# Optimization experiments

Hardware: AMD Instinct MI355X
Metric: run time of the kernel (lower is better)

## Reference

```python
import jax, jax.numpy as jnp
import numpy as np

# Allpass biquad coefficients (torchaudio.functional.allpass_biquad semantics)
SAMPLE_RATE = 16000
CENTRAL_FREQ = 4000.0
Q = 0.707

def _allpass_coeffs(sample_rate, central_freq, q):
    w0 = 2.0 * np.pi * central_freq / sample_rate
    alpha = np.sin(w0) / (2.0 * q)
    cos_w0 = np.cos(w0)
    b0 = 1.0 - alpha
    b1 = -2.0 * cos_w0
    b2 = 1.0 + alpha
    a0 = 1.0 + alpha
    a1 = -2.0 * cos_w0
    a2 = 1.0 - alpha
    # normalize by a0 (as torchaudio.biquad does)
    return (np.float32(b0 / a0), np.float32(b1 / a0), np.float32(b2 / a0),
            np.float32(a1 / a0), np.float32(a2 / a0))

B0, B1, B2, A1, A2 = _allpass_coeffs(SAMPLE_RATE, CENTRAL_FREQ, Q)


def setup_inputs() -> dict:
    key = jax.random.key(0)
    x = jax.random.normal(key, (64, 1, 480000), dtype=jnp.float32)
    return {"x": x}


def _biquad(x):
    # x: [B, 1, T] -> y: [B, 1, T]
    B, C, T = x.shape
    xt = jnp.transpose(x[:, 0, :])  # [T, B] for time-major scan

    def step(carry, xn):
        x1, x2, y1, y2 = carry
        yn = B0 * xn + B1 * x1 + B2 * x2 - A1 * y1 - A2 * y2
        return (xn, x1, yn, y1), yn

    z = jnp.zeros((B,), dtype=x.dtype)
    _, yt = jax.lax.scan(step, (z, z, z, z), xt)
    return jnp.transpose(yt)[:, None, :]  # back to [B, 1, T]


def reference(x):
    return _biquad(x)
```

## Files before the change

kernel.cpp:

```cpp
#include <hip/hip_runtime.h>
#include <cmath>

#define T_LEN   480000
#define BATCH   64
#define CHUNK   16
#define WARM    32
#define TPB     256
#define TS      (TPB * CHUNK)
#define TPR     ((T_LEN + TS - 1) / TS)
#define NLOAD_MAX (TS + WARM)
#define LDS_SLOTS (NLOAD_MAX + ((NLOAD_MAX >> 5) << 2))

__device__ __forceinline__ int slot4(int i) { return i + ((i >> 5) << 2); }

#define STEP(XN, YN)                                            \
    {                                                           \
        float u_ = fmaf(B0, (XN), fmaf(B1, x1, B2 * x2));       \
        (YN) = fmaf(-A1, y1, fmaf(-A2, y2, u_));                \
        x2 = x1; x1 = (XN); y2 = y1; y1 = (YN);                 \
    }

__global__ __launch_bounds__(TPB) void allpass_kernel(
    const float* __restrict__ x, float* __restrict__ y,
    float B0, float B1, float B2, float A1, float A2)
{
    __shared__ __align__(16) float lds[LDS_SLOTS];
    const int tid  = threadIdx.x;
    const int row  = blockIdx.x / TPR;
    const int tb   = blockIdx.x % TPR;
    const int sbase = tb * TS;
    const int ns   = min(TS, T_LEN - sbase);
    const float* __restrict__ xr = x + (size_t)row * T_LEN + sbase;
    float* __restrict__ yr       = y + (size_t)row * T_LEN + sbase;

    const int nload = ns + WARM;
    for (int i4 = tid * 4; i4 < nload; i4 += TPB * 4) {
        float4 v;
        if (tb == 0 && i4 < WARM) {
            v = make_float4(0.f, 0.f, 0.f, 0.f);
        } else {
            v = *(const float4*)(xr - WARM + i4);
        }
        *(float4*)&lds[slot4(i4)] = v;
    }
    __syncthreads();

    float4 yq[CHUNK / 4];
    const int ls = tid * CHUNK;
    const bool active = (ls < ns);
    if (active) {
        float x1 = 0.f, x2 = 0.f, y1 = 0.f, y2 = 0.f;
        #pragma unroll
        for (int t4 = 0; t4 < WARM; t4 += 4) {
            float4 xv = *(const float4*)&lds[slot4(ls + t4)];
            float t;
            STEP(xv.x, t); STEP(xv.y, t); STEP(xv.z, t); STEP(xv.w, t);
        }
        #pragma unroll
        for (int t4 = 0; t4 < CHUNK; t4 += 4) {
            float4 xv = *(const float4*)&lds[slot4(ls + WARM + t4)];
            float4 yv;
            STEP(xv.x, yv.x); STEP(xv.y, yv.y);
            STEP(xv.z, yv.z); STEP(xv.w, yv.w);
            yq[t4 / 4] = yv;
        }
    }
    __syncthreads();

    if (active) {
        #pragma unroll
        for (int t4 = 0; t4 < CHUNK; t4 += 4)
            *(float4*)&lds[slot4(ls + t4)] = yq[t4 / 4];
    }
    __syncthreads();

    for (int i4 = tid * 4; i4 < ns; i4 += TPB * 4) {
        float4 v = *(const float4*)&lds[slot4(i4)];
        *(float4*)(yr + i4) = v;
    }
}

extern "C" void kernel_launch(void* const* d_in, const int* in_sizes, int n_in,
                              void* d_out, int out_size, void* d_ws, size_t ws_size,
                              hipStream_t stream) {
    const float* x = (const float*)d_in[0];
    float* y = (float*)d_out;

    const double sample_rate = 16000.0, central_freq = 4000.0, Q = 0.707;
    const double w0 = 2.0 * M_PI * central_freq / sample_rate;
    const double alpha = sin(w0) / (2.0 * Q);
    const double cw = cos(w0);
    const double a0 = 1.0 + alpha;
    const float B0 = (float)((1.0 - alpha) / a0);
    const float B1 = (float)((-2.0 * cw) / a0);
    const float B2 = (float)((1.0 + alpha) / a0);
    const float A1 = (float)((-2.0 * cw) / a0);
    const float A2 = (float)((1.0 - alpha) / a0);

    const int blocks = BATCH * TPR;
    allpass_kernel<<<blocks, TPB, 0, stream>>>(x, y, B0, B1, B2, A1, A2);
}
```

Baseline: 216.4 us.

## Halve warm-up length, batch global loads, store outputs directly to global

```diff
diff --git a/kernel.cpp b/kernel.cpp
--- a/kernel.cpp
+++ b/kernel.cpp
@@ -4,11 +4,12 @@
 #define T_LEN   480000
 #define BATCH   64
 #define CHUNK   16
-#define WARM    32
+#define WARM    16
 #define TPB     256
 #define TS      (TPB * CHUNK)
 #define TPR     ((T_LEN + TS - 1) / TS)
 #define NLOAD_MAX (TS + WARM)
+#define NITER   ((NLOAD_MAX + TPB * 4 - 1) / (TPB * 4))
 #define LDS_SLOTS (NLOAD_MAX + ((NLOAD_MAX >> 5) << 2))
 
 __device__ __forceinline__ int slot4(int i) { return i + ((i >> 5) << 2); }
@@ -32,23 +33,29 @@
     const int ns   = min(TS, T_LEN - sbase);
     const float* __restrict__ xr = x + (size_t)row * T_LEN + sbase;
     float* __restrict__ yr       = y + (size_t)row * T_LEN + sbase;
+    const int nload = ns + WARM;
 
-    const int nload = ns + WARM;
-    for (int i4 = tid * 4; i4 < nload; i4 += TPB * 4) {
-        float4 v;
-        if (tb == 0 && i4 < WARM) {
-            v = make_float4(0.f, 0.f, 0.f, 0.f);
-        } else {
-            v = *(const float4*)(xr - WARM + i4);
+    float4 vbuf[NITER];
+    #pragma unroll
+    for (int j = 0; j < NITER; ++j) {
+        const int i4 = tid * 4 + j * (TPB * 4);
+        if (i4 < nload) {
+            if (tb == 0 && i4 < WARM)
+                vbuf[j] = make_float4(0.f, 0.f, 0.f, 0.f);
+            else
+                vbuf[j] = *(const float4*)(xr - WARM + i4);
         }
-        *(float4*)&lds[slot4(i4)] = v;
+    }
+    #pragma unroll
+    for (int j = 0; j < NITER; ++j) {
+        const int i4 = tid * 4 + j * (TPB * 4);
+        if (i4 < nload)
+            *(float4*)&lds[slot4(i4)] = vbuf[j];
     }
     __syncthreads();
 
-    float4 yq[CHUNK / 4];
     const int ls = tid * CHUNK;
-    const bool active = (ls < ns);
-    if (active) {
+    if (ls < ns) {
         float x1 = 0.f, x2 = 0.f, y1 = 0.f, y2 = 0.f;
         #pragma unroll
         for (int t4 = 0; t4 < WARM; t4 += 4) {
@@ -62,21 +69,8 @@
             float4 yv;
             STEP(xv.x, yv.x); STEP(xv.y, yv.y);
             STEP(xv.z, yv.z); STEP(xv.w, yv.w);
-            yq[t4 / 4] = yv;
+            *(float4*)(yr + ls + t4) = yv;
         }
-    }
-    __syncthreads();
-
-    if (active) {
-        #pragma unroll
-        for (int t4 = 0; t4 < CHUNK; t4 += 4)
-            *(float4*)&lds[slot4(ls + t4)] = yq[t4 / 4];
-    }
-    __syncthreads();
-
-    for (int i4 = tid * 4; i4 < ns; i4 += TPB * 4) {
-        float4 v = *(const float4*)&lds[slot4(i4)];
-        *(float4*)(yr + i4) = v;
     }
 }
 
```

Measured after the change: 218.6 us. No clear change (+1.0%).
